# Optimization experiments

Hardware: AMD Instinct MI355X
Metric: run time of the kernel (lower is better)

The kernel has to match this reference:

```python
import jax, jax.numpy as jnp
import numpy as np

GROUPS = 32
EPS = 1e-5


def group_norm(x, gamma, beta):
    b, h, w, c = x.shape
    xg = x.reshape(b, h, w, GROUPS, c // GROUPS)
    mean = jnp.mean(xg, axis=(1, 2, 4), keepdims=True)
    var = jnp.var(xg, axis=(1, 2, 4), keepdims=True)
    xn = ((xg - mean) * jax.lax.rsqrt(var + EPS)).reshape(b, h, w, c)
    return xn * gamma + beta


def conv1x1(x, w, b):
    # 1x1 conv == per-pixel dense: [b,h,w,c] x [c,d] -> [b,h,w,d]
    return jnp.einsum('bhwc,cd->bhwd', x, w) + b


def setup_inputs() -> dict:
    key = jax.random.key(0)
    ks = jax.random.split(key, 6)
    B, H, W, C = 4, 64, 64, 512
    s = 1.0 / np.sqrt(C)
    return {
        'x': jax.random.normal(ks[0], (B, H, W, C), jnp.float32),
        'gn_gamma': jnp.ones((C,), jnp.float32),
        'gn_beta': jnp.zeros((C,), jnp.float32),
        'wq': jax.random.normal(ks[1], (C, C), jnp.float32) * s,
        'bq': jnp.zeros((C,), jnp.float32),
        'wk': jax.random.normal(ks[2], (C, C), jnp.float32) * s,
        'bk': jnp.zeros((C,), jnp.float32),
        'wv': jax.random.normal(ks[3], (C, C), jnp.float32) * s,
        'bv': jnp.zeros((C,), jnp.float32),
        'wp': jax.random.normal(ks[4], (C, C), jnp.float32) * s,
        'bp': jnp.zeros((C,), jnp.float32),
    }


def reference(x, gn_gamma, gn_beta, wq, bq, wk, bk, wv, bv, wp, bp):
    b, h, w, c = x.shape
    n = h * w
    h_ = group_norm(x, gn_gamma, gn_beta)
    q = conv1x1(h_, wq, bq).reshape(b, n, c)
    k = conv1x1(h_, wk, bk).reshape(b, n, c)
    v = conv1x1(h_, wv, bv).reshape(b, n, c)
    scale = c ** (-0.5)
    scores = jnp.einsum('bic,bjc->bij', q, k) * scale  # [b, n, n]
    attn = jax.nn.softmax(scores, axis=-1)
    out = jnp.einsum('bij,bjc->bic', attn, v).reshape(b, h, w, c)
    return x + conv1x1(out, wp, bp)
```

## Files before the change

### kernel.cpp

```cpp
#include <hip/hip_runtime.h>
#include <cstdint>


typedef __bf16 bf16_t;
typedef bf16_t bf16x8 __attribute__((ext_vector_type(8)));
typedef float floatx4 __attribute__((ext_vector_type(4)));
typedef int v8i __attribute__((ext_vector_type(8)));

__device__ __forceinline__ uint16_t f2b(float f) {
    uint32_t u = __builtin_bit_cast(uint32_t, f);
    u += 0x7fffu + ((u >> 16) & 1u);
    return (uint16_t)(u >> 16);
}
__device__ __forceinline__ float b2f(uint16_t h) {
    uint32_t u = ((uint32_t)h) << 16;
    return __builtin_bit_cast(float, u);
}
__device__ __forceinline__ unsigned pk_fp8x4(float a, float b, float c, float d) {
    int w = __builtin_amdgcn_cvt_pk_fp8_f32(a, b, 0, false);
    w = __builtin_amdgcn_cvt_pk_fp8_f32(c, d, w, true);
    return (unsigned)w;
}

__device__ __forceinline__ void lds_copy16(void* lds, const void* glob) {
    __builtin_amdgcn_global_load_lds(
        (__attribute__((address_space(1))) void*)(void*)glob,
        (__attribute__((address_space(3))) void*)lds,
        16, 0, 0);
}

__global__ __launch_bounds__(256) void gn_stats(const float* __restrict__ x,
                                                float* __restrict__ stats,
                                                float* __restrict__ lrow) {
    const int bg = blockIdx.x;
    const int tid = threadIdx.x;
    if (tid < 128) lrow[bg * 128 + tid] = 0.f;
    const int b = bg >> 5, g = bg & 31;
    const float* base = x + (long)b * (4096L * 512) + g * 16;
    float s = 0.f, sq = 0.f;
    #pragma unroll 8
    for (int i = 0; i < 64; i++) {
        int idx4 = tid + i * 256;
        int pixel = idx4 >> 2, c4 = idx4 & 3;
        const float4 v = *(const float4*)(base + (long)pixel * 512 + c4 * 4);
        s += v.x + v.y + v.z + v.w;
        sq += v.x * v.x + v.y * v.y + v.z * v.z + v.w * v.w;
    }
    #pragma unroll
    for (int off = 32; off > 0; off >>= 1) {
        s += __shfl_down(s, off);
        sq += __shfl_down(sq, off);
    }
    __shared__ float rs[4], rq[4];
    const int lane = tid & 63, w = tid >> 6;
    if (lane == 0) { rs[w] = s; rq[w] = sq; }
    __syncthreads();
    if (tid == 0) {
        float S = rs[0] + rs[1] + rs[2] + rs[3];
        float Q = rq[0] + rq[1] + rq[2] + rq[3];
        float mean = S * (1.f / 65536.f);
        float var = Q * (1.f / 65536.f) - mean * mean;
        stats[bg * 2 + 0] = mean;
        stats[bg * 2 + 1] = rsqrtf(var + 1e-5f);
    }
}

__global__ __launch_bounds__(256) void gn_apply(const float* __restrict__ x,
                                                const float* __restrict__ stats,
                                                const float* __restrict__ gamma,
                                                const float* __restrict__ beta,
                                                uint16_t* __restrict__ h) {
    const long idx4 = (long)blockIdx.x * 256 + threadIdx.x;
    const long e0 = idx4 * 4;
    const int c = (int)(e0 & 511);
    const int b = (int)(e0 >> 21);
    const float2 st = ((const float2*)stats)[b * 32 + (c >> 4)];
    const float4 v = ((const float4*)x)[idx4];
    const float4 gm = ((const float4*)gamma)[c >> 2];
    const float4 bt = ((const float4*)beta)[c >> 2];
    union { ushort4 u; uint16_t s[4]; } o;
    o.s[0] = f2b((v.x - st.x) * st.y * gm.x + bt.x);
    o.s[1] = f2b((v.y - st.x) * st.y * gm.y + bt.y);
    o.s[2] = f2b((v.z - st.x) * st.y * gm.z + bt.z);
    o.s[3] = f2b((v.w - st.x) * st.y * gm.w + bt.w);
    ((ushort4*)h)[idx4] = o.u;
}

__global__ __launch_bounds__(256) void wcast_transpose(const float* __restrict__ w0,
                                                       const float* __restrict__ w1,
                                                       const float* __restrict__ w2,
                                                       const float* __restrict__ w3,
                                                       uint16_t* __restrict__ out) {
    const float* ws[4] = {w0, w1, w2, w3};
    const float* w = ws[blockIdx.z];
    uint16_t* o = out + (long)blockIdx.z * 512 * 512;
    __shared__ uint16_t t[64][65];
    const int nb = blockIdx.x * 64, kb = blockIdx.y * 64;
    const int lc = threadIdx.x & 63, lg = threadIdx.x >> 6;
    #pragma unroll
    for (int i = 0; i < 16; i++) {
        int r = lg * 16 + i;
        t[lc][r] = f2b(w[(long)(kb + r) * 512 + nb + lc]);
    }
    __syncthreads();
    #pragma unroll
    for (int i = 0; i < 16; i++) {
        int r = lg * 16 + i;
        o[(long)(nb + r) * 512 + kb + lc] = t[r][lc];
    }
}

__global__ __launch_bounds__(256) void qkv_gemm(const uint16_t* __restrict__ h,
                                                const uint16_t* __restrict__ wT,
                                                const float* __restrict__ bq,
                                                const float* __restrict__ bk,
                                                const float* __restrict__ bv,
                                                uint8_t* __restrict__ q,
                                                uint8_t* __restrict__ k,
                                                uint8_t* __restrict__ vt) {
    __shared__ __align__(16) uint16_t smem[128 * 136];
    uint16_t* sA = smem;
    uint16_t* sB = smem + 8192;

    const int tid = threadIdx.x;
    const long m0 = (long)blockIdx.y * 128;
    const int n0 = blockIdx.x * 128;

    const int lane = tid & 63;
    const int wave = tid >> 6;
    const int wm = (wave & 1) * 64;
    const int wn = (wave >> 1) * 64;
    const int fr = lane & 15;
    const int fh = lane >> 4;
    const int sw = fr & 7;

    floatx4 acc[4][4];
    #pragma unroll
    for (int i = 0; i < 4; i++)
        #pragma unroll
        for (int j = 0; j < 4; j++) acc[i][j] = (floatx4){0.f, 0.f, 0.f, 0.f};

    for (int kt = 0; kt < 512; kt += 64) {
        __syncthreads();
        #pragma unroll
        for (int i = 0; i < 4; i++) {
            const int c = i * 256 + tid;
            const int row = c >> 3;
            const int gj = (c & 7) ^ (row & 7);
            lds_copy16(&sA[c * 8], h + (m0 + row) * 512L + kt + gj * 8);
            lds_copy16(&sB[c * 8], wT + (n0 + row) * 512L + kt + gj * 8);
        }
        __syncthreads();
        #pragma unroll
        for (int kk = 0; kk < 64; kk += 32) {
            const int jx = ((fh + (kk >> 3)) ^ sw) * 8;
            bf16x8 av[4], bv_[4];
            #pragma unroll
            for (int mi = 0; mi < 4; mi++)
                av[mi] = *(const bf16x8*)&sA[(wm + mi * 16 + fr) * 64 + jx];
            #pragma unroll
            for (int ni = 0; ni < 4; ni++)
                bv_[ni] = *(const bf16x8*)&sB[(wn + ni * 16 + fr) * 64 + jx];
            #pragma unroll
            for (int mi = 0; mi < 4; mi++)
                #pragma unroll
                for (int ni = 0; ni < 4; ni++)
                    acc[mi][ni] = __builtin_amdgcn_mfma_f32_16x16x32_bf16(
                        av[mi], bv_[ni], acc[mi][ni], 0, 0, 0);
        }
    }

    const int quad = lane >> 4;
    const int w = n0 >> 9;
    const int nc = n0 & 511;
    const float* bias = (w == 0) ? bq : (w == 1) ? bk : bv;
    __syncthreads();
    if (w < 2) {
        #pragma unroll
        for (int ni = 0; ni < 4; ni++) {
            const int col_l = wn + ni * 16 + fr;
            const float bb = bias[nc + col_l];
            #pragma unroll
            for (int mi = 0; mi < 4; mi++) {
                #pragma unroll
                for (int r = 0; r < 4; r++) {
                    const int row_l = wm + mi * 16 + quad * 4 + r;
                    smem[row_l * 136 + col_l] = f2b(acc[mi][ni][r] + bb);
                }
            }
        }
        __syncthreads();
        uint8_t* out = (w == 0) ? q : k;
        #pragma unroll
        for (int it = 0; it < 8; it++) {
            const int row_l = it * 16 + (tid >> 4);
            const int c0 = (tid & 15) * 8;
            const uint4 d = *(const uint4*)&smem[row_l * 136 + c0];
            const uint16_t* e = (const uint16_t*)&d;
            uint2 o;
            o.x = pk_fp8x4(b2f(e[0]), b2f(e[1]), b2f(e[2]), b2f(e[3]));
            o.y = pk_fp8x4(b2f(e[4]), b2f(e[5]), b2f(e[6]), b2f(e[7]));
            *(uint2*)&out[(m0 + row_l) * 512 + nc + c0] = o;
        }
    } else {
        uint8_t* s8 = (uint8_t*)smem;
        #pragma unroll
        for (int ni = 0; ni < 4; ni++) {
            const int ch_l = wn + ni * 16 + fr;
            const float bb = bias[nc + ch_l];
            #pragma unroll
            for (int mi = 0; mi < 4; mi++) {
                const int pix0 = wm + mi * 16 + quad * 4;
                *(unsigned*)&s8[ch_l * 144 + pix0] =
                    pk_fp8x4(acc[mi][ni][0] + bb, acc[mi][ni][1] + bb,
                             acc[mi][ni][2] + bb, acc[mi][ni][3] + bb);
            }
        }
        __syncthreads();
        const long b = m0 >> 12;
        const int pixb = (int)(m0 & 4095);
        uint8_t* vtb = vt + b * (512L * 4096);
        #pragma unroll
        for (int it = 0; it < 4; it++) {
            const int ch_l = it * 32 + (tid >> 3);
            const int p0 = (tid & 7) * 16;
            *(uint4*)&vtb[(long)(nc + ch_l) * 4096 + pixb + p0] =
                *(const uint4*)&s8[ch_l * 144 + p0];
        }
    }
}

template <int MODE>
__global__ __launch_bounds__(256) void gemm_f8(const uint8_t* __restrict__ A,
                                               const uint8_t* __restrict__ B,
                                               void* __restrict__ Cout,
                                               float* __restrict__ lrow,
                                               float scale, int M, int N, int K,
                                               long aStride, long bStride, long cStride) {
    __shared__ __align__(16) uint16_t smem[128 * 136];
    __shared__ float lbuf[128];
    uint8_t* sA = (uint8_t*)smem;
    uint8_t* sB = (uint8_t*)smem + 16384;

    const int tid = threadIdx.x;
    const int bz = blockIdx.z;
    const long m0 = (long)blockIdx.y * 128;
    const long n0 = (long)blockIdx.x * 128;
    const uint8_t* Ab = A + (long)bz * aStride;
    const uint8_t* Bb = B + (long)bz * bStride;

    const int lane = tid & 63;
    const int wave = tid >> 6;
    const int wm = (wave & 1) * 64;
    const int wn = (wave >> 1) * 64;
    const int fr = lane & 15;
    const int quad = lane >> 4;
    const int sw = fr & 7;

    floatx4 acc[4][4];
    #pragma unroll
    for (int i = 0; i < 4; i++)
        #pragma unroll
        for (int j = 0; j < 4; j++) acc[i][j] = (floatx4){0.f, 0.f, 0.f, 0.f};

    const int p0c = (2 * quad) ^ sw;
    const int p1c = (2 * quad + 1) ^ sw;

    for (int kt = 0; kt < K; kt += 128) {
        __syncthreads();
        #pragma unroll
        for (int i = 0; i < 4; i++) {
            const int c = i * 256 + tid;
            const int row = c >> 3;
            const int gj = (c & 7) ^ (row & 7);
            lds_copy16(&sA[c * 16], Ab + (m0 + row) * (long)K + kt + gj * 16);
            lds_copy16(&sB[c * 16], Bb + (n0 + row) * (long)K + kt + gj * 16);
        }
        __syncthreads();
        v8i af[4], bf[4];
        #pragma unroll
        for (int mi = 0; mi < 4; mi++) {
            const int row = wm + mi * 16 + fr;
            const uint4 lo = *(const uint4*)&sA[row * 128 + p0c * 16];
            const uint4 hi = *(const uint4*)&sA[row * 128 + p1c * 16];
            af[mi] = (v8i){(int)lo.x, (int)lo.y, (int)lo.z, (int)lo.w,
                           (int)hi.x, (int)hi.y, (int)hi.z, (int)hi.w};
        }
        #pragma unroll
        for (int ni = 0; ni < 4; ni++) {
            const int row = wn + ni * 16 + fr;
            const uint4 lo = *(const uint4*)&sB[row * 128 + p0c * 16];
            const uint4 hi = *(const uint4*)&sB[row * 128 + p1c * 16];
            bf[ni] = (v8i){(int)lo.x, (int)lo.y, (int)lo.z, (int)lo.w,
                           (int)hi.x, (int)hi.y, (int)hi.z, (int)hi.w};
        }
        #pragma unroll
        for (int mi = 0; mi < 4; mi++)
            #pragma unroll
            for (int ni = 0; ni < 4; ni++)
                acc[mi][ni] = __builtin_amdgcn_mfma_scale_f32_16x16x128_f8f6f4(
                    af[mi], bf[ni], acc[mi][ni], 0, 0,
                    0, 0x7f7f7f7fu, 0, 0x7f7f7f7fu);
    }

    __syncthreads();
    if (MODE == 4) {
        if (tid < 128) lbuf[tid] = lrow[(long)bz * M + m0 + tid];
        __syncthreads();
    }
    #pragma unroll
    for (int ni = 0; ni < 4; ni++) {
        const int col_l = wn + ni * 16 + fr;
        #pragma unroll
        for (int mi = 0; mi < 4; mi++) {
            #pragma unroll
            for (int r = 0; r < 4; r++) {
                const int row_l = wm + mi * 16 + quad * 4 + r;
                float v = acc[mi][ni][r];
                if (MODE == 3) v = exp2f(v * scale);
                if (MODE == 4) v *= __builtin_amdgcn_rcpf(lbuf[row_l]);
                smem[row_l * 136 + col_l] = f2b(v);
            }
        }
    }
    __syncthreads();
    if (MODE == 3) {
        uint8_t* Cb = (uint8_t*)Cout + (long)bz * cStride;
        float* lb = lrow + (long)bz * M;
        #pragma unroll
        for (int it = 0; it < 8; it++) {
            const int row_l = it * 16 + (tid >> 4);
            const int c0 = (tid & 15) * 8;
            const uint4 d = *(const uint4*)&smem[row_l * 136 + c0];
            const uint16_t* e = (const uint16_t*)&d;
            float f[8];
            float ps = 0.f;
            #pragma unroll
            for (int j = 0; j < 8; j++) { f[j] = b2f(e[j]); ps += f[j]; }
            uint2 o;
            o.x = pk_fp8x4(f[0], f[1], f[2], f[3]);
            o.y = pk_fp8x4(f[4], f[5], f[6], f[7]);
            *(uint2*)&Cb[(m0 + row_l) * (long)N + n0 + c0] = o;
            #pragma unroll
            for (int off = 1; off < 16; off <<= 1) ps += __shfl_xor(ps, off);
            if ((tid & 15) == 0) atomicAdd(&lb[m0 + row_l], ps);
        }
    } else {
        uint16_t* Cb = (uint16_t*)Cout + (long)bz * cStride;
        #pragma unroll
        for (int it = 0; it < 8; it++) {
            const int row_l = it * 16 + (tid >> 4);
            const int c0 = (tid & 15) * 8;
            *(uint4*)&Cb[(m0 + row_l) * (long)N + n0 + c0] =
                *(const uint4*)&smem[row_l * 136 + c0];
        }
    }
}

__global__ __launch_bounds__(256) void gemm_proj(const uint16_t* __restrict__ A,
                                                 const uint16_t* __restrict__ B,
                                                 float* __restrict__ Cout,
                                                 const float* __restrict__ bias,
                                                 const float* __restrict__ resid) {
    __shared__ __align__(16) uint16_t smem[128 * 136];
    uint16_t* sA = smem;
    uint16_t* sB = smem + 8192;
    const int N = 512;

    const int tid = threadIdx.x;
    const long m0 = (long)blockIdx.y * 128;
    const long n0 = (long)blockIdx.x * 128;

    const int lane = tid & 63;
    const int wave = tid >> 6;
    const int wm = (wave & 1) * 64;
    const int wn = (wave >> 1) * 64;
    const int fr = lane & 15;
    const int fh = lane >> 4;
    const int sw = fr & 7;

    floatx4 acc[4][4];
    #pragma unroll
    for (int i = 0; i < 4; i++)
        #pragma unroll
        for (int j = 0; j < 4; j++) acc[i][j] = (floatx4){0.f, 0.f, 0.f, 0.f};

    for (int kt = 0; kt < 512; kt += 64) {
        __syncthreads();
        #pragma unroll
        for (int i = 0; i < 4; i++) {
            const int c = i * 256 + tid;
            const int row = c >> 3;
            const int gj = (c & 7) ^ (row & 7);
            lds_copy16(&sA[c * 8], A + (m0 + row) * 512L + kt + gj * 8);
            lds_copy16(&sB[c * 8], B + (n0 + row) * 512L + kt + gj * 8);
        }
        __syncthreads();
        #pragma unroll
        for (int kk = 0; kk < 64; kk += 32) {
            const int jx = ((fh + (kk >> 3)) ^ sw) * 8;
            bf16x8 av[4], bv[4];
            #pragma unroll
            for (int mi = 0; mi < 4; mi++)
                av[mi] = *(const bf16x8*)&sA[(wm + mi * 16 + fr) * 64 + jx];
            #pragma unroll
            for (int ni = 0; ni < 4; ni++)
                bv[ni] = *(const bf16x8*)&sB[(wn + ni * 16 + fr) * 64 + jx];
            #pragma unroll
            for (int mi = 0; mi < 4; mi++)
                #pragma unroll
                for (int ni = 0; ni < 4; ni++)
                    acc[mi][ni] = __builtin_amdgcn_mfma_f32_16x16x32_bf16(
                        av[mi], bv[ni], acc[mi][ni], 0, 0, 0);
        }
    }

    const int quad = lane >> 4;
    #pragma unroll
    for (int ni = 0; ni < 4; ni++) {
        const long col = n0 + wn + ni * 16 + fr;
        const float bv_ = bias[col];
        #pragma unroll
        for (int mi = 0; mi < 4; mi++) {
            #pragma unroll
            for (int r = 0; r < 4; r++) {
                const long row = m0 + wm + mi * 16 + quad * 4 + r;
                Cout[row * N + col] = acc[mi][ni][r] + bv_ + resid[row * N + col];
            }
        }
    }
}

extern "C" void kernel_launch(void* const* d_in, const int* in_sizes, int n_in,
                              void* d_out, int out_size, void* d_ws, size_t ws_size,
                              hipStream_t stream) {
    const float* x  = (const float*)d_in[0];
    const float* gg = (const float*)d_in[1];
    const float* gb = (const float*)d_in[2];
    const float* wq = (const float*)d_in[3];
    const float* bq = (const float*)d_in[4];
    const float* wk = (const float*)d_in[5];
    const float* bk = (const float*)d_in[6];
    const float* wv = (const float*)d_in[7];
    const float* bv = (const float*)d_in[8];
    const float* wp = (const float*)d_in[9];
    const float* bp = (const float*)d_in[10];
    float* out = (float*)d_out;

    char* ws = (char*)d_ws;
    size_t off = 0;
    auto alloc = [&](size_t bytes) {
        char* p = ws + off;
        off += (bytes + 255) & ~(size_t)255;
        return p;
    };
    float*    stats = (float*)alloc(128 * 2 * sizeof(float));
    float*    lrow  = (float*)alloc(16384L * 4);
    uint16_t* h     = (uint16_t*)alloc(16384L * 512 * 2);
    uint16_t* wT    = (uint16_t*)alloc(4L * 512 * 512 * 2);
    uint8_t*  q8    = (uint8_t*)alloc(16384L * 512);
    uint8_t*  k8    = (uint8_t*)alloc(16384L * 512);
    uint8_t*  vt8   = (uint8_t*)alloc(16384L * 512);
    uint8_t*  sc8   = (uint8_t*)alloc(4L * 4096 * 4096);
    uint16_t* ao    = (uint16_t*)alloc(16384L * 512 * 2);
    if (off > ws_size) return;

    gn_stats<<<128, 256, 0, stream>>>(x, stats, lrow);
    gn_apply<<<8192, 256, 0, stream>>>(x, stats, gg, gb, h);
    wcast_transpose<<<dim3(8, 8, 4), 256, 0, stream>>>(wq, wk, wv, wp, wT);

    qkv_gemm<<<dim3(12, 128), 256, 0, stream>>>(h, wT, bq, bk, bv, q8, k8, vt8);
    const float qscale = 0.06375871540654937f;
    gemm_f8<3><<<dim3(32, 32, 4), 256, 0, stream>>>(q8, k8, sc8, lrow, qscale,
                                                    4096, 4096, 512,
                                                    4096L * 512, 4096L * 512, 4096L * 4096);
    gemm_f8<4><<<dim3(4, 32, 4), 256, 0, stream>>>(sc8, vt8, ao, lrow, 1.f,
                                                   4096, 512, 4096,
                                                   4096L * 4096, 512L * 4096, 4096L * 512);
    gemm_proj<<<dim3(4, 128), 256, 0, stream>>>(ao, wT + 3 * 262144, out, bp, x);
}
```

Before: 313.4 us.

## Fuse QK^T, exp, row-sum and PV into a single flash-attention kernel

Replaces the two-pass attention (write an fp8 score matrix to global memory, then a second GEMM that reads it back and normalizes) with one fused kernel. Each block holds a 64-row Q tile in registers, streams K and V^T from global memory, computes exp2 scores, stages them as fp8 in LDS for the PV MFMA, and normalizes by the accumulated row sums at the end. This removes the 64 MB score round-trip through global memory, the atomics and the lrow zeroing. In exchange, K and V are read directly from global without LDS staging, and the grid is only 256 blocks, so GPU occupancy is limited. Like the old code, there is no max-subtraction in the softmax.

```diff
diff --git a/kernel.cpp b/kernel.cpp
--- a/kernel.cpp
+++ b/kernel.cpp
@@ -30,11 +30,9 @@
 }
 
 __global__ __launch_bounds__(256) void gn_stats(const float* __restrict__ x,
-                                                float* __restrict__ stats,
-                                                float* __restrict__ lrow) {
+                                                float* __restrict__ stats) {
     const int bg = blockIdx.x;
     const int tid = threadIdx.x;
-    if (tid < 128) lrow[bg * 128 + tid] = 0.f;
     const int b = bg >> 5, g = bg & 31;
     const float* base = x + (long)b * (4096L * 512) + g * 16;
     float s = 0.f, sq = 0.f;
@@ -230,130 +228,185 @@
     }
 }
 
-template <int MODE>
-__global__ __launch_bounds__(256) void gemm_f8(const uint8_t* __restrict__ A,
-                                               const uint8_t* __restrict__ B,
-                                               void* __restrict__ Cout,
-                                               float* __restrict__ lrow,
-                                               float scale, int M, int N, int K,
-                                               long aStride, long bStride, long cStride) {
-    __shared__ __align__(16) uint16_t smem[128 * 136];
-    __shared__ float lbuf[128];
-    uint8_t* sA = (uint8_t*)smem;
-    uint8_t* sB = (uint8_t*)smem + 16384;
+__global__ __launch_bounds__(512, 2) void flash_attn(const uint8_t* __restrict__ q8,
+                                                     const uint8_t* __restrict__ k8,
+                                                     const uint8_t* __restrict__ vt8,
+                                                     uint16_t* __restrict__ ao) {
+    __shared__ __align__(16) uint8_t Pl[64 * 128];
+    __shared__ float lpart[8][16];
+    __shared__ float linv[64];
+    __shared__ __align__(16) uint16_t obuf[64 * 256];
 
     const int tid = threadIdx.x;
-    const int bz = blockIdx.z;
-    const long m0 = (long)blockIdx.y * 128;
-    const long n0 = (long)blockIdx.x * 128;
-    const uint8_t* Ab = A + (long)bz * aStride;
-    const uint8_t* Bb = B + (long)bz * bStride;
-
     const int lane = tid & 63;
     const int wave = tid >> 6;
-    const int wm = (wave & 1) * 64;
-    const int wn = (wave >> 1) * 64;
     const int fr = lane & 15;
     const int quad = lane >> 4;
-    const int sw = fr & 7;
-
-    floatx4 acc[4][4];
+
+    const int lb = ((blockIdx.x & 7) << 5) | (blockIdx.x >> 3);
+    const int batch = lb >> 6;
+    const int mt = lb & 63;
+    const long qbase = (long)batch * 4096 + mt * 64;
+
+    const int wm = (wave >> 1) * 16;
+    const int wc = (wave & 1) * 64;
+    const float qscale = 0.06375871540654937f;
+
+    v8i aQ[4];
+    {
+        const uint8_t* qp = q8 + (qbase + wm + fr) * 512 + quad * 32;
+        #pragma unroll
+        for (int kt = 0; kt < 4; kt++) {
+            const uint4 lo = *(const uint4*)(qp + kt * 128);
+            const uint4 hi = *(const uint4*)(qp + kt * 128 + 16);
+            aQ[kt] = (v8i){(int)lo.x, (int)lo.y, (int)lo.z, (int)lo.w,
+                           (int)hi.x, (int)hi.y, (int)hi.z, (int)hi.w};
+        }
+    }
+    const uint8_t* krow = k8 + (long)batch * (4096L * 512) +
+                          (long)(wc + fr) * 512 + quad * 32;
+    const uint8_t* vrow = vt8 + (long)batch * (512L * 4096) +
+                          (long)(wave * 64 + fr) * 4096 + quad * 32;
+
+    floatx4 oacc[4][4];
     #pragma unroll
     for (int i = 0; i < 4; i++)
         #pragma unroll
-        for (int j = 0; j < 4; j++) acc[i][j] = (floatx4){0.f, 0.f, 0.f, 0.f};
-
-    const int p0c = (2 * quad) ^ sw;
-    const int p1c = (2 * quad + 1) ^ sw;
-
-    for (int kt = 0; kt < K; kt += 128) {
-        __syncthreads();
-        #pragma unroll
-        for (int i = 0; i < 4; i++) {
-            const int c = i * 256 + tid;
-            const int row = c >> 3;
-            const int gj = (c & 7) ^ (row & 7);
-            lds_copy16(&sA[c * 16], Ab + (m0 + row) * (long)K + kt + gj * 16);
-            lds_copy16(&sB[c * 16], Bb + (n0 + row) * (long)K + kt + gj * 16);
-        }
-        __syncthreads();
-        v8i af[4], bf[4];
+        for (int j = 0; j < 4; j++) oacc[i][j] = (floatx4){0.f, 0.f, 0.f, 0.f};
+    float lsum[4] = {0.f, 0.f, 0.f, 0.f};
+
+#define LOADK(dst, kt_)                                                        \
+    do {                                                                       \
+        _Pragma("unroll")                                                      \
+        for (int ni = 0; ni < 4; ni++) {                                       \
+            const uint8_t* kp = ktb + (long)ni * (16L * 512) + (kt_) * 128;    \
+            const uint4 lo = *(const uint4*)kp;                                \
+            const uint4 hi = *(const uint4*)(kp + 16);                         \
+            dst[ni] = (v8i){(int)lo.x, (int)lo.y, (int)lo.z, (int)lo.w,        \
+                            (int)hi.x, (int)hi.y, (int)hi.z, (int)hi.w};       \
+        }                                                                      \
+    } while (0)
+
+#define SSTEP(kt_, bK)                                                         \
+    do {                                                                       \
+        _Pragma("unroll")                                                      \
+        for (int ni = 0; ni < 4; ni++)                                         \
+            sacc[ni] = __builtin_amdgcn_mfma_scale_f32_16x16x128_f8f6f4(       \
+                aQ[kt_], bK[ni], sacc[ni], 0, 0, 0, 0x7f7f7f7fu, 0,            \
+                0x7f7f7f7fu);                                                  \
+    } while (0)
+
+    for (int t = 0; t < 32; t++) {
+        const uint8_t* ktb = krow + (long)t * (128L * 512);
+        floatx4 sacc[4];
+        #pragma unroll
+        for (int ni = 0; ni < 4; ni++) sacc[ni] = (floatx4){0.f, 0.f, 0.f, 0.f};
+        {
+            v8i bKa[4], bKb[4];
+            LOADK(bKa, 0);
+            LOADK(bKb, 1);
+            SSTEP(0, bKa);
+            LOADK(bKa, 2);
+            SSTEP(1, bKb);
+            LOADK(bKb, 3);
+            SSTEP(2, bKa);
+            SSTEP(3, bKb);
+        }
+        v8i bV[4];
+        #pragma unroll
+        for (int ni = 0; ni < 4; ni++) {
+            const uint8_t* vp = vrow + (long)ni * (16L * 4096) + t * 128;
+            const uint4 lo = *(const uint4*)vp;
+            const uint4 hi = *(const uint4*)(vp + 16);
+            bV[ni] = (v8i){(int)lo.x, (int)lo.y, (int)lo.z, (int)lo.w,
+                           (int)hi.x, (int)hi.y, (int)hi.z, (int)hi.w};
+        }
+        unsigned pk[4];
+        #pragma unroll
+        for (int ni = 0; ni < 4; ni++) {
+            const float p0 = exp2f(sacc[ni][0] * qscale);
+            const float p1 = exp2f(sacc[ni][1] * qscale);
+            const float p2 = exp2f(sacc[ni][2] * qscale);
+            const float p3 = exp2f(sacc[ni][3] * qscale);
+            lsum[0] += p0;
+            lsum[1] += p1;
+            lsum[2] += p2;
+            lsum[3] += p3;
+            pk[ni] = pk_fp8x4(p0, p1, p2, p3);
+        }
+        __syncthreads();
+        #pragma unroll
+        for (int ni = 0; ni < 4; ni++) {
+            const int chunk = ((wave & 1) << 2) | ni;
+            #pragma unroll
+            for (int r = 0; r < 4; r++) {
+                const int prow = wm + quad * 4 + r;
+                Pl[prow * 128 + ((chunk ^ (prow & 7)) << 4) + fr] =
+                    (uint8_t)(pk[ni] >> (8 * r));
+            }
+        }
+        __syncthreads();
         #pragma unroll
         for (int mi = 0; mi < 4; mi++) {
-            const int row = wm + mi * 16 + fr;
-            const uint4 lo = *(const uint4*)&sA[row * 128 + p0c * 16];
-            const uint4 hi = *(const uint4*)&sA[row * 128 + p1c * 16];
-            af[mi] = (v8i){(int)lo.x, (int)lo.y, (int)lo.z, (int)lo.w,
-                           (int)hi.x, (int)hi.y, (int)hi.z, (int)hi.w};
-        }
-        #pragma unroll
-        for (int ni = 0; ni < 4; ni++) {
-            const int row = wn + ni * 16 + fr;
-            const uint4 lo = *(const uint4*)&sB[row * 128 + p0c * 16];
-            const uint4 hi = *(const uint4*)&sB[row * 128 + p1c * 16];
-            bf[ni] = (v8i){(int)lo.x, (int)lo.y, (int)lo.z, (int)lo.w,
-                           (int)hi.x, (int)hi.y, (int)hi.z, (int)hi.w};
-        }
-        #pragma unroll
-        for (int mi = 0; mi < 4; mi++)
+            const int prow = mi * 16 + fr;
+            const int sw8 = fr & 7;
+            const uint4 lo = *(const uint4*)&Pl[prow * 128 + (((2 * quad) ^ sw8) << 4)];
+            const uint4 hi = *(const uint4*)&Pl[prow * 128 + (((2 * quad + 1) ^ sw8) << 4)];
+            const v8i aP = (v8i){(int)lo.x, (int)lo.y, (int)lo.z, (int)lo.w,
+                                 (int)hi.x, (int)hi.y, (int)hi.z, (int)hi.w};
             #pragma unroll
             for (int ni = 0; ni < 4; ni++)
-                acc[mi][ni] = __builtin_amdgcn_mfma_scale_f32_16x16x128_f8f6f4(
-                    af[mi], bf[ni], acc[mi][ni], 0, 0,
-                    0, 0x7f7f7f7fu, 0, 0x7f7f7f7fu);
-    }
-
+                oacc[mi][ni] = __builtin_amdgcn_mfma_scale_f32_16x16x128_f8f6f4(
+                    aP, bV[ni], oacc[mi][ni], 0, 0, 0, 0x7f7f7f7fu, 0,
+                    0x7f7f7f7fu);
+        }
+    }
+#undef LOADK
+#undef SSTEP
+
+    #pragma unroll
+    for (int r = 0; r < 4; r++) {
+        #pragma unroll
+        for (int off = 1; off < 16; off <<= 1)
+            lsum[r] += __shfl_xor(lsum[r], off);
+    }
+    if ((lane & 15) == 0) {
+        #pragma unroll
+        for (int r = 0; r < 4; r++) lpart[wave][quad * 4 + r] = lsum[r];
+    }
     __syncthreads();
-    if (MODE == 4) {
-        if (tid < 128) lbuf[tid] = lrow[(long)bz * M + m0 + tid];
-        __syncthreads();
-    }
-    #pragma unroll
-    for (int ni = 0; ni < 4; ni++) {
-        const int col_l = wn + ni * 16 + fr;
-        #pragma unroll
-        for (int mi = 0; mi < 4; mi++) {
-            #pragma unroll
-            for (int r = 0; r < 4; r++) {
-                const int row_l = wm + mi * 16 + quad * 4 + r;
-                float v = acc[mi][ni][r];
-                if (MODE == 3) v = exp2f(v * scale);
-                if (MODE == 4) v *= __builtin_amdgcn_rcpf(lbuf[row_l]);
-                smem[row_l * 136 + col_l] = f2b(v);
-            }
-        }
+    if (tid < 64) {
+        const int j = tid >> 4;
+        const float L = lpart[2 * j][tid & 15] + lpart[2 * j + 1][tid & 15];
+        linv[tid] = __builtin_amdgcn_rcpf(L);
     }
     __syncthreads();
-    if (MODE == 3) {
-        uint8_t* Cb = (uint8_t*)Cout + (long)bz * cStride;
-        float* lb = lrow + (long)bz * M;
-        #pragma unroll
-        for (int it = 0; it < 8; it++) {
-            const int row_l = it * 16 + (tid >> 4);
-            const int c0 = (tid & 15) * 8;
-            const uint4 d = *(const uint4*)&smem[row_l * 136 + c0];
-            const uint16_t* e = (const uint16_t*)&d;
-            float f[8];
-            float ps = 0.f;
-            #pragma unroll
-            for (int j = 0; j < 8; j++) { f[j] = b2f(e[j]); ps += f[j]; }
-            uint2 o;
-            o.x = pk_fp8x4(f[0], f[1], f[2], f[3]);
-            o.y = pk_fp8x4(f[4], f[5], f[6], f[7]);
-            *(uint2*)&Cb[(m0 + row_l) * (long)N + n0 + c0] = o;
-            #pragma unroll
-            for (int off = 1; off < 16; off <<= 1) ps += __shfl_xor(ps, off);
-            if ((tid & 15) == 0) atomicAdd(&lb[m0 + row_l], ps);
-        }
-    } else {
-        uint16_t* Cb = (uint16_t*)Cout + (long)bz * cStride;
-        #pragma unroll
-        for (int it = 0; it < 8; it++) {
-            const int row_l = it * 16 + (tid >> 4);
-            const int c0 = (tid & 15) * 8;
-            *(uint4*)&Cb[(m0 + row_l) * (long)N + n0 + c0] =
-                *(const uint4*)&smem[row_l * 136 + c0];
-        }
+    #pragma unroll
+    for (int hh = 0; hh < 2; hh++) {
+        if ((wave >> 2) == hh) {
+            #pragma unroll
+            for (int mi = 0; mi < 4; mi++)
+                #pragma unroll
+                for (int ni = 0; ni < 4; ni++)
+                    #pragma unroll
+                    for (int r = 0; r < 4; r++) {
+                        const int row = mi * 16 + quad * 4 + r;
+                        const int col = (wave & 3) * 64 + ni * 16 + fr;
+                        obuf[row * 256 + col] = f2b(oacc[mi][ni][r] * linv[row]);
+                    }
+        }
+        __syncthreads();
+        {
+            const int srow = tid >> 3;
+            const int sc = tid & 7;
+            uint16_t* dst = ao + (qbase + srow) * 512 + hh * 256;
+            const uint16_t* src = &obuf[srow * 256];
+            #pragma unroll
+            for (int it = 0; it < 4; it++)
+                *(uint4*)(dst + (sc + it * 8) * 8) =
+                    *(const uint4*)(src + (sc + it * 8) * 8);
+        }
+        __syncthreads();
     }
 }
 
@@ -455,27 +508,19 @@
         return p;
     };
     float*    stats = (float*)alloc(128 * 2 * sizeof(float));
-    float*    lrow  = (float*)alloc(16384L * 4);
     uint16_t* h     = (uint16_t*)alloc(16384L * 512 * 2);
     uint16_t* wT    = (uint16_t*)alloc(4L * 512 * 512 * 2);
     uint8_t*  q8    = (uint8_t*)alloc(16384L * 512);
     uint8_t*  k8    = (uint8_t*)alloc(16384L * 512);
     uint8_t*  vt8   = (uint8_t*)alloc(16384L * 512);
-    uint8_t*  sc8   = (uint8_t*)alloc(4L * 4096 * 4096);
     uint16_t* ao    = (uint16_t*)alloc(16384L * 512 * 2);
     if (off > ws_size) return;
 
-    gn_stats<<<128, 256, 0, stream>>>(x, stats, lrow);
+    gn_stats<<<128, 256, 0, stream>>>(x, stats);
     gn_apply<<<8192, 256, 0, stream>>>(x, stats, gg, gb, h);
     wcast_transpose<<<dim3(8, 8, 4), 256, 0, stream>>>(wq, wk, wv, wp, wT);
 
     qkv_gemm<<<dim3(12, 128), 256, 0, stream>>>(h, wT, bq, bk, bv, q8, k8, vt8);
-    const float qscale = 0.06375871540654937f;
-    gemm_f8<3><<<dim3(32, 32, 4), 256, 0, stream>>>(q8, k8, sc8, lrow, qscale,
-                                                    4096, 4096, 512,
-                                                    4096L * 512, 4096L * 512, 4096L * 4096);
-    gemm_f8<4><<<dim3(4, 32, 4), 256, 0, stream>>>(sc8, vt8, ao, lrow, 1.f,
-                                                   4096, 512, 4096,
-                                                   4096L * 4096, 512L * 4096, 4096L * 512);
+    flash_attn<<<dim3(256), dim3(512), 0, stream>>>(q8, k8, vt8, ao);
     gemm_proj<<<dim3(4, 128), 256, 0, stream>>>(ao, wT + 3 * 262144, out, bp, x);
 }
```

After: 496.6 us. +58.5%, slower.
